# Kernel tuning notes

Hardware: AMD Instinct MI355X
Metric: run time of the kernel (lower is better)

Reference implementation:

```python
import jax, jax.numpy as jnp
import numpy as np

HID = 256
SLOTS = 64
K = 2
TAU = 8.0
EPS = 1e-5


def setup_inputs() -> dict:
    key = jax.random.key(0)
    ks = jax.random.split(key, 8)
    B, T = 512, 256
    s = lambda fan_in: 1.0 / np.sqrt(fan_in)
    return {
        "x": jax.random.uniform(ks[0], (B, T, 1), jnp.float32, 0.0, 10.0),
        "W_embed": jax.random.uniform(ks[1], (HID, 1), jnp.float32, -1.0, 1.0),
        "b_embed": jax.random.uniform(ks[2], (HID,), jnp.float32, -1.0, 1.0),
        "W_update": jax.random.uniform(ks[3], (HID, HID), jnp.float32, -s(HID), s(HID)),
        "b_update": jax.random.uniform(ks[4], (HID,), jnp.float32, -s(HID), s(HID)),
        "gamma": jnp.ones((HID,), jnp.float32),
        "beta": jnp.zeros((HID,), jnp.float32),
        "W_out": jax.random.uniform(ks[5], (10, HID), jnp.float32, -s(HID), s(HID)),
        "b_out": jax.random.uniform(ks[6], (10,), jnp.float32, -s(HID), s(HID)),
        "context_strength": jnp.float32(0.2),
    }


def _gaussian_attention(pointer, num_positions):
    # pointer: [B] float. Returns indices [B,5] int32, weights [B,5] float.
    offsets = jnp.arange(-K, K + 1)
    base = jnp.clip(jnp.floor(pointer).astype(jnp.int32), 0, num_positions - 1)
    indices = (base[:, None] + offsets[None, :]) % num_positions
    delta = indices.astype(pointer.dtype) - pointer[:, None]
    weights = jax.nn.softmax(-(delta ** 2) / TAU, axis=1)
    return indices, weights


def reference(x, W_embed, b_embed, W_update, b_update, gamma, beta, W_out, b_out, context_strength):
    B, T, _ = x.shape
    cs = jax.nn.sigmoid(context_strength)

    def step(carry, x_t):
        h, memory, pointer = carry  # [B,H], [B,SLOTS,H], [B]
        inp = jnp.tanh(x_t @ W_embed.T + b_embed)           # [B,H]
        indices, weights = _gaussian_attention(pointer, SLOTS)
        neighborhood = jnp.take_along_axis(memory, indices[:, :, None], axis=1)  # [B,5,H]
        context = jnp.einsum('bk,bkh->bh', weights, neighborhood)
        combined = inp + cs * context
        h = jnp.tanh((combined + h) @ W_update.T + b_update)
        mu = jnp.mean(h, axis=-1, keepdims=True)
        var = jnp.mean((h - mu) ** 2, axis=-1, keepdims=True)
        h = (h - mu) * jax.lax.rsqrt(var + EPS) * gamma + beta
        contribution = weights[:, :, None] * h[:, None, :]   # [B,5,H]
        memory = jax.vmap(lambda m, i, c: m.at[i].add(c))(memory, indices, contribution)
        pointer = (pointer + 1.0) % SLOTS
        return (h, memory, pointer), None

    h0 = jnp.zeros((B, HID), x.dtype)
    mem0 = jnp.zeros((B, SLOTS, HID), x.dtype)
    ptr0 = jnp.zeros((B,), x.dtype)
    (h, _, _), _ = jax.lax.scan(step, (h0, mem0, ptr0), jnp.swapaxes(x, 0, 1))
    return h @ W_out.T + b_out
```

## Files before the change

kernel.cpp:

```cpp
#include <hip/hip_runtime.h>


#define TT 256

typedef __bf16 bf16x8 __attribute__((ext_vector_type(8)));
typedef float  f32x4  __attribute__((ext_vector_type(4)));

__device__ __forceinline__ float fast_tanh(float x) {
    float e = __expf(2.f * x);
    return 1.f - __fdividef(2.f, e + 1.f);
}

template<int CTRL, int RM>
__device__ __forceinline__ float dpp_add(float v) {
    int t = __builtin_amdgcn_update_dpp(0, __float_as_int(v), CTRL, RM, 0xf, true);
    return v + __int_as_float(t);
}
__device__ __forceinline__ float swap32_add(float v) {
    float a = v, b = v;
    asm("v_permlane32_swap_b32 %0, %1" : "+v"(a), "+v"(b));
    return a + b;
}

#define SMEM_BYTES 136656

__global__ __launch_bounds__(512, 2)
void postnorm_kernel(const float* __restrict__ x,
                     const float* __restrict__ W_embed,
                     const float* __restrict__ b_embed,
                     const float* __restrict__ W_update,
                     const float* __restrict__ b_update,
                     const float* __restrict__ gamma,
                     const float* __restrict__ beta,
                     const float* __restrict__ W_out,
                     const float* __restrict__ b_out,
                     const float* __restrict__ ctx_s,
                     float* __restrict__ out)
{
    extern __shared__ __align__(16) char smem[];
    float*  s_mem  = (float*)(smem);
    float*  s_x    = (float*)(smem + 131072);
    __bf16* s_v    = (__bf16*)(smem + 133120);
    float*  s_red1 = (float*)(smem + 134272);
    float*  s_red2 = (float*)(smem + 134400);
    float*  s_wt   = (float*)(smem + 134528);
    float*  s_oacc = (float*)(smem + 136576);

    const int tid  = threadIdx.x;
    const int wave = tid >> 6;
    const int lane = tid & 63;
    const int bn   = lane & 15;
    const int quad = lane >> 4;
    const int r0   = blockIdx.x * 2;

    const int b     = bn >> 1;
    const int row   = bn & 1;
    const int i_own = wave * 32 + (b >> 2) * 16 + quad * 4 + (b & 3);

    {   f32x4 z = {0.f, 0.f, 0.f, 0.f};
        f32x4* p = (f32x4*)s_mem;
        #pragma unroll
        for (int k = 0; k < 16; ++k) p[tid + k * 512] = z;
    }
    s_x[tid] = x[(r0 + (tid >> 8)) * TT + (tid & 255)];
    if (tid < 64) ((float*)(smem + 134272))[tid] = 0.f;
    if (tid < 20) s_oacc[tid] = 0.f;

    if (tid < 64) {
        float wv[5]; float ssum = 0.f;
        #pragma unroll
        for (int k = 0; k < 5; ++k) {
            int idx = (tid + k - 2) & 63;
            float d = (float)idx - (float)tid;
            wv[k] = expf(-(d * d) * 0.125f);
            ssum += wv[k];
        }
        #pragma unroll
        for (int k = 0; k < 5; ++k) s_wt[tid * 8 + k] = wv[k] / ssum;
    }

    const float we  = W_embed[i_own];
    const float be  = b_embed[i_own];
    const float bu  = b_update[i_own];
    const float gm  = gamma[i_own];
    const float btt = beta[i_own];
    const float csv = 1.f / (1.f + expf(-ctx_s[0]));

    bf16x8 wfa[2][8];
    #pragma unroll
    for (int mt = 0; mt < 2; ++mt) {
        #pragma unroll
        for (int kt = 0; kt < 8; ++kt) {
            const float* wp = W_update + (wave * 32 + mt * 16 + bn) * 256
                                       + kt * 32 + quad * 8;
            f32x4 a = *(const f32x4*)wp;
            f32x4 bb = *(const f32x4*)(wp + 4);
            bf16x8 f;
            f[0] = (__bf16)a[0];  f[1] = (__bf16)a[1];
            f[2] = (__bf16)a[2];  f[3] = (__bf16)a[3];
            f[4] = (__bf16)bb[0]; f[5] = (__bf16)bb[1];
            f[6] = (__bf16)bb[2]; f[7] = (__bf16)bb[3];
            wfa[mt][kt] = f;
        }
    }

    __syncthreads();
    {
        float inp0 = fast_tanh(s_x[row * 256] * we + be);
        s_v[row * 288 + i_own] = (__bf16)inp0;
    }

    float wt0, wt1, wt2, wt3, wt4;
    {   f32x4 wv = *(const f32x4*)(s_wt);
        wt0 = wv[0]; wt1 = wv[1]; wt2 = wv[2]; wt3 = wv[3]; wt4 = s_wt[4];
    }
    f32x4 nw  = *(const f32x4*)(s_wt + 8);
    float nw4 = s_wt[8 + 4];
    float xn  = s_x[row * 256 + 1];
    float nf  = 0.f;
    __syncthreads();

    float hn = 0.f;
    float w0 = 0.f, w1 = 0.f, w2 = 0.f, w3 = 0.f, w4 = 0.f;
    float* mcol = s_mem + (row << 14) + i_own;
    const __bf16* vsrc = s_v + row * 288 + quad * 8;

    #pragma unroll 1
    for (int t = 0; t < TT; ++t) {
        float inp = fast_tanh(xn * we + be);

        f32x4 a0a = {0,0,0,0}, a0b = {0,0,0,0}, a1a = {0,0,0,0}, a1b = {0,0,0,0};
        #pragma unroll
        for (int kt = 0; kt < 4; ++kt) {
            bf16x8 bfr0 = *(const bf16x8*)(vsrc + kt * 32);
            bf16x8 bfr1 = *(const bf16x8*)(vsrc + (kt + 4) * 32);
            a0a = __builtin_amdgcn_mfma_f32_16x16x32_bf16(wfa[0][kt],     bfr0, a0a, 0, 0, 0);
            a1a = __builtin_amdgcn_mfma_f32_16x16x32_bf16(wfa[1][kt],     bfr0, a1a, 0, 0, 0);
            a0b = __builtin_amdgcn_mfma_f32_16x16x32_bf16(wfa[0][kt + 4], bfr1, a0b, 0, 0, 0);
            a1b = __builtin_amdgcn_mfma_f32_16x16x32_bf16(wfa[1][kt + 4], bfr1, a1b, 0, 0, 0);
        }

        f32x4 y0 = a0a + a0b, y1 = a1a + a1b;
        f32x4 ym = (b & 4) ? y1 : y0;
        float yA = (b & 2) ? ym[2] : ym[0];
        float yB = (b & 2) ? ym[3] : ym[1];
        float ysel = (b & 1) ? yB : yA;

        float yt = fast_tanh(ysel + bu);
        float s1 = yt, s2 = yt * yt;
        s1 = dpp_add<0x4E,  0xf>(s1);  s2 = dpp_add<0x4E,  0xf>(s2);
        s1 = dpp_add<0x124, 0xf>(s1);  s2 = dpp_add<0x124, 0xf>(s2);
        s1 = dpp_add<0x128, 0xf>(s1);  s2 = dpp_add<0x128, 0xf>(s2);
        s1 = swap32_add(s1);           s2 = swap32_add(s2);
        if ((lane & 46) == 0) {
            const int b4 = (lane >> 4) & 1;
            s_red1[(lane & 1) * 16 + wave * 2 + b4] = s1;
            s_red2[(lane & 1) * 16 + wave * 2 + b4] = s2;
        }
        __syncthreads();

        const float* rp1 = s_red1 + row * 16;
        const float* rp2 = s_red2 + row * 16;
        f32x4 r1a = *(const f32x4*)rp1,       r1b = *(const f32x4*)(rp1 + 4);
        f32x4 r1c = *(const f32x4*)(rp1 + 8), r1d = *(const f32x4*)(rp1 + 12);
        f32x4 r2a = *(const f32x4*)rp2,       r2b = *(const f32x4*)(rp2 + 4);
        f32x4 r2c = *(const f32x4*)(rp2 + 8), r2d = *(const f32x4*)(rp2 + 12);
        float S1 = (((r1a[0]+r1a[1]) + (r1a[2]+r1a[3])) + ((r1b[0]+r1b[1]) + (r1b[2]+r1b[3])))
                 + (((r1c[0]+r1c[1]) + (r1c[2]+r1c[3])) + ((r1d[0]+r1d[1]) + (r1d[2]+r1d[3])));
        float S2 = (((r2a[0]+r2a[1]) + (r2a[2]+r2a[3])) + ((r2b[0]+r2b[1]) + (r2b[2]+r2b[3])))
                 + (((r2c[0]+r2c[1]) + (r2c[2]+r2c[3])) + ((r2d[0]+r2d[1]) + (r2d[2]+r2d[3])));
        float mu   = S1 * (1.f / 256.f);
        float var  = S2 * (1.f / 256.f) - mu * mu;
        float rstd = rsqrtf(var + 1e-5f);
        hn = (yt - mu) * rstd * gm + btt;

        w0 += wt0 * hn; w1 += wt1 * hn; w2 += wt2 * hn;
        w3 += wt3 * hn; w4 += wt4 * hn;

        mcol[((t - 2) & 63) << 8] = w0;
        w0 = w1; w1 = w2; w2 = w3; w3 = w4; w4 = nf;
        float ctx = ((nw[0] * w0 + nw[1] * w1) + (nw[2] * w2 + nw[3] * w3))
                  + nw4 * w4;
        float v = inp + csv * ctx + hn;
        s_v[row * 288 + i_own] = (__bf16)v;
        wt0 = nw[0]; wt1 = nw[1]; wt2 = nw[2]; wt3 = nw[3]; wt4 = nw4;

        nf  = mcol[((t + 4) & 63) << 8];
        {   const float* wp = s_wt + ((t + 2) & 63) * 8;
            nw  = *(const f32x4*)wp;
            nw4 = wp[4];
        }
        xn  = s_x[row * 256 + ((t + 2) & 255)];
        __syncthreads();
    }

    s_x[row * 256 + i_own] = hn;
    __syncthreads();
    {
        const int n = tid >> 8, i = tid & 255;
        float h = s_x[tid];
        #pragma unroll
        for (int o = 0; o < 10; ++o) {
            float p = h * W_out[o * 256 + i];
            #pragma unroll
            for (int m = 32; m >= 1; m >>= 1) p += __shfl_xor(p, m, 64);
            if (lane == 0) atomicAdd(&s_oacc[n * 10 + o], p);
        }
    }
    __syncthreads();
    if (tid < 20) {
        int nn = tid / 10, o = tid % 10;
        out[(r0 + nn) * 10 + o] = s_oacc[tid] + b_out[o];
    }
}

extern "C" void kernel_launch(void* const* d_in, const int* in_sizes, int n_in,
                              void* d_out, int out_size, void* d_ws, size_t ws_size,
                              hipStream_t stream) {
    const float* x    = (const float*)d_in[0];
    const float* W_e  = (const float*)d_in[1];
    const float* b_e  = (const float*)d_in[2];
    const float* W_u  = (const float*)d_in[3];
    const float* b_u  = (const float*)d_in[4];
    const float* gmm  = (const float*)d_in[5];
    const float* bta  = (const float*)d_in[6];
    const float* W_o  = (const float*)d_in[7];
    const float* b_o  = (const float*)d_in[8];
    const float* cst  = (const float*)d_in[9];
    float* out = (float*)d_out;

    (void)hipFuncSetAttribute(reinterpret_cast<const void*>(postnorm_kernel),
                              hipFuncAttributeMaxDynamicSharedMemorySize,
                              SMEM_BYTES);

    postnorm_kernel<<<dim3(256), dim3(512), SMEM_BYTES, stream>>>(
        x, W_e, b_e, W_u, b_u, gmm, bta, W_o, b_o, cst, out);
}
```

Before: 313.8 us.

## Shorten per-step critical path: precompute context before GEMM, atomic LDS norm reduction

The context dot product and the coefficient on hn are now computed before the MFMA, using an algebraic split (ctx = ctxA + wdot*hn). This leaves only a couple of FMAs after the layer norm on the serial recurrence. The tanh inputs are pre-scaled by 2/ln2 so exp2 can be used directly. The cross-wave LayerNorm sum now does a full in-wave reduction with a permlane16 swap and LDS atomicAdd into a double-buffered 8-float accumulator, replacing the 16-value reads and adds per row. In exchange it adds LDS atomic contention across 8 waves and changes the float summation order.

New measurement: 295.7 us. 1.06x faster.

```diff
diff --git a/kernel.cpp b/kernel.cpp
--- a/kernel.cpp
+++ b/kernel.cpp
@@ -5,9 +5,12 @@
 
 typedef __bf16 bf16x8 __attribute__((ext_vector_type(8)));
 typedef float  f32x4  __attribute__((ext_vector_type(4)));
-
-__device__ __forceinline__ float fast_tanh(float x) {
-    float e = __expf(2.f * x);
+typedef float  f32x2  __attribute__((ext_vector_type(2)));
+
+#define C2 2.8853900817779268f
+
+__device__ __forceinline__ float tanh_pre(float u) {
+    float e = exp2f(u);
     return 1.f - __fdividef(2.f, e + 1.f);
 }
 
@@ -21,8 +24,13 @@
     asm("v_permlane32_swap_b32 %0, %1" : "+v"(a), "+v"(b));
     return a + b;
 }
-
-#define SMEM_BYTES 136656
+__device__ __forceinline__ float swap16_add(float v) {
+    float a = v, b = v;
+    asm("v_permlane16_swap_b32 %0, %1" : "+v"(a), "+v"(b));
+    return a + b;
+}
+
+#define SMEM_BYTES 136432
 
 __global__ __launch_bounds__(512, 2)
 void postnorm_kernel(const float* __restrict__ x,
@@ -41,10 +49,9 @@
     float*  s_mem  = (float*)(smem);
     float*  s_x    = (float*)(smem + 131072);
     __bf16* s_v    = (__bf16*)(smem + 133120);
-    float*  s_red1 = (float*)(smem + 134272);
-    float*  s_red2 = (float*)(smem + 134400);
-    float*  s_wt   = (float*)(smem + 134528);
-    float*  s_oacc = (float*)(smem + 136576);
+    float*  s_acc  = (float*)(smem + 134272);
+    float*  s_wt   = (float*)(smem + 134304);
+    float*  s_oacc = (float*)(smem + 136352);
 
     const int tid  = threadIdx.x;
     const int wave = tid >> 6;
@@ -63,7 +70,7 @@
         for (int k = 0; k < 16; ++k) p[tid + k * 512] = z;
     }
     s_x[tid] = x[(r0 + (tid >> 8)) * TT + (tid & 255)];
-    if (tid < 64) ((float*)(smem + 134272))[tid] = 0.f;
+    if (tid < 8)  s_acc[tid] = 0.f;
     if (tid < 20) s_oacc[tid] = 0.f;
 
     if (tid < 64) {
@@ -79,9 +86,9 @@
         for (int k = 0; k < 5; ++k) s_wt[tid * 8 + k] = wv[k] / ssum;
     }
 
-    const float we  = W_embed[i_own];
-    const float be  = b_embed[i_own];
-    const float bu  = b_update[i_own];
+    const float we2 = W_embed[i_own] * C2;
+    const float be2 = b_embed[i_own] * C2;
+    const float bu2 = b_update[i_own] * C2;
     const float gm  = gamma[i_own];
     const float btt = beta[i_own];
     const float csv = 1.f / (1.f + expf(-ctx_s[0]));
@@ -106,7 +113,7 @@
 
     __syncthreads();
     {
-        float inp0 = fast_tanh(s_x[row * 256] * we + be);
+        float inp0 = tanh_pre(fmaf(s_x[row * 256], we2, be2));
         s_v[row * 288 + i_own] = (__bf16)inp0;
     }
 
@@ -127,7 +134,14 @@
 
     #pragma unroll 1
     for (int t = 0; t < TT; ++t) {
-        float inp = fast_tanh(xn * we + be);
+        const int rb = t & 1, wb = rb ^ 1;
+
+        float inp  = tanh_pre(fmaf(xn, we2, be2));
+        float ctxA = ((nw[0] * w1 + nw[1] * w2) + (nw[2] * w3 + nw[3] * w4))
+                   + nw4 * nf;
+        float wdot = (nw[0] * wt1 + nw[1] * wt2) + (nw[2] * wt3 + nw[3] * wt4);
+        float base = fmaf(csv, ctxA, inp);
+        float coef = fmaf(csv, wdot, 1.f);
 
         f32x4 a0a = {0,0,0,0}, a0b = {0,0,0,0}, a1a = {0,0,0,0}, a1b = {0,0,0,0};
         #pragma unroll
@@ -146,45 +160,32 @@
         float yB = (b & 2) ? ym[3] : ym[1];
         float ysel = (b & 1) ? yB : yA;
 
-        float yt = fast_tanh(ysel + bu);
+        float yt = tanh_pre(fmaf(ysel, C2, bu2));
         float s1 = yt, s2 = yt * yt;
         s1 = dpp_add<0x4E,  0xf>(s1);  s2 = dpp_add<0x4E,  0xf>(s2);
         s1 = dpp_add<0x124, 0xf>(s1);  s2 = dpp_add<0x124, 0xf>(s2);
         s1 = dpp_add<0x128, 0xf>(s1);  s2 = dpp_add<0x128, 0xf>(s2);
+        s1 = swap16_add(s1);           s2 = swap16_add(s2);
         s1 = swap32_add(s1);           s2 = swap32_add(s2);
-        if ((lane & 46) == 0) {
-            const int b4 = (lane >> 4) & 1;
-            s_red1[(lane & 1) * 16 + wave * 2 + b4] = s1;
-            s_red2[(lane & 1) * 16 + wave * 2 + b4] = s2;
-        }
+        if (lane < 4)
+            atomicAdd(&s_acc[rb * 4 + (lane & 1) * 2 + (lane >> 1)],
+                      (lane & 2) ? s2 : s1);
         __syncthreads();
 
-        const float* rp1 = s_red1 + row * 16;
-        const float* rp2 = s_red2 + row * 16;
-        f32x4 r1a = *(const f32x4*)rp1,       r1b = *(const f32x4*)(rp1 + 4);
-        f32x4 r1c = *(const f32x4*)(rp1 + 8), r1d = *(const f32x4*)(rp1 + 12);
-        f32x4 r2a = *(const f32x4*)rp2,       r2b = *(const f32x4*)(rp2 + 4);
-        f32x4 r2c = *(const f32x4*)(rp2 + 8), r2d = *(const f32x4*)(rp2 + 12);
-        float S1 = (((r1a[0]+r1a[1]) + (r1a[2]+r1a[3])) + ((r1b[0]+r1b[1]) + (r1b[2]+r1b[3])))
-                 + (((r1c[0]+r1c[1]) + (r1c[2]+r1c[3])) + ((r1d[0]+r1d[1]) + (r1d[2]+r1d[3])));
-        float S2 = (((r2a[0]+r2a[1]) + (r2a[2]+r2a[3])) + ((r2b[0]+r2b[1]) + (r2b[2]+r2b[3])))
-                 + (((r2c[0]+r2c[1]) + (r2c[2]+r2c[3])) + ((r2d[0]+r2d[1]) + (r2d[2]+r2d[3])));
-        float mu   = S1 * (1.f / 256.f);
-        float var  = S2 * (1.f / 256.f) - mu * mu;
+        f32x2 S = *(const f32x2*)(s_acc + rb * 4 + row * 2);
+        if (tid < 4) s_acc[wb * 4 + tid] = 0.f;
+        float mu   = S[0] * (1.f / 256.f);
+        float var  = S[1] * (1.f / 256.f) - mu * mu;
         float rstd = rsqrtf(var + 1e-5f);
-        hn = (yt - mu) * rstd * gm + btt;
+        hn = fmaf(yt - mu, rstd * gm, btt);
+        float v = fmaf(coef, hn, base);
+        s_v[row * 288 + i_own] = (__bf16)v;
 
         w0 += wt0 * hn; w1 += wt1 * hn; w2 += wt2 * hn;
         w3 += wt3 * hn; w4 += wt4 * hn;
-
         mcol[((t - 2) & 63) << 8] = w0;
         w0 = w1; w1 = w2; w2 = w3; w3 = w4; w4 = nf;
-        float ctx = ((nw[0] * w0 + nw[1] * w1) + (nw[2] * w2 + nw[3] * w3))
-                  + nw4 * w4;
-        float v = inp + csv * ctx + hn;
-        s_v[row * 288 + i_own] = (__bf16)v;
         wt0 = nw[0]; wt1 = nw[1]; wt2 = nw[2]; wt3 = nw[3]; wt4 = nw4;
-
         nf  = mcol[((t + 4) & 63) << 8];
         {   const float* wp = s_wt + ((t + 2) & 63) * 8;
             nw  = *(const f32x4*)wp;
```
